# Kernel optimization log

Measured on AMD Instinct MI355X. Metric: run time of the kernel, lower is better.

## Reference

```python
import jax, jax.numpy as jnp
import numpy as np

B, C, D, H, W = 2, 96, 32, 64, 64
K = 2            # MRConv stride
EPS = 1e-5
SLOPE = 0.2      # LeakyReLU negative slope used by ViG act_layer('leakyrelu')


def conv1x1(x, w, b):
    # 1x1x1 Conv3d == per-voxel channel GEMM. x: [B,Ci,D,H,W], w: [Co,Ci]
    return jnp.einsum('bcdhw,oc->bodhw', x, w) + b[None, :, None, None, None]


def batchnorm(x, g, b):
    # training-mode BatchNorm3d: stats over (B, D, H, W)
    m = x.mean(axis=(0, 2, 3, 4), keepdims=True)
    v = x.var(axis=(0, 2, 3, 4), keepdims=True)
    return (x - m) * jax.lax.rsqrt(v + EPS) * g[None, :, None, None, None] + b[None, :, None, None, None]


def instnorm(x, g, b):
    # InstanceNorm3d: stats over (D, H, W) per sample/channel
    m = x.mean(axis=(2, 3, 4), keepdims=True)
    v = x.var(axis=(2, 3, 4), keepdims=True)
    return (x - m) * jax.lax.rsqrt(v + EPS) * g[None, :, None, None, None] + b[None, :, None, None, None]


def lrelu(x):
    return jnp.where(x >= 0, x, SLOPE * x)


def mr_aggregate(x):
    # MRConv shift/subtract/max, in closed form.
    # Original: x_j = max over axes a, shifts s in range(K, L_a, K) of (x - roll(x, s, a)), init 0.
    # Since shifts cover ALL nonzero multiples of K mod L_a (L_a % K == 0), the rolled values at a
    # position are exactly the other members of its residue class mod K along that axis, and
    # max(0, x - min_excluding_self) == x - min_including_self.  Hence:
    #   x_j = x - min over axes of (strided residue-class min along that axis).
    def axmin(x, axis):
        L = x.shape[axis]
        shp = list(x.shape)
        grp = shp[:axis] + [L // K, K] + shp[axis + 1:]
        xg = x.reshape(grp)
        m = xg.min(axis=axis, keepdims=True)             # min over same residue class
        return jnp.broadcast_to(m, grp).reshape(shp)
    m = jnp.minimum(jnp.minimum(axmin(x, 2), axmin(x, 3)), axmin(x, 4))
    return x - m


def setup_inputs() -> dict:
    key = jax.random.key(0)
    ks = jax.random.split(key, 8)
    f32 = jnp.float32
    def w(k, co, ci):
        return (jax.random.normal(k, (co, ci), dtype=f32) / np.sqrt(ci)).astype(f32)
    return {
        'x': jax.random.normal(ks[0], (B, C, D, H, W), dtype=f32),
        'w_fc1': w(ks[1], C, C), 'b_fc1': jnp.zeros((C,), f32),
        'g_bn1': jnp.ones((C,), f32), 'be_bn1': jnp.zeros((C,), f32),
        'w_g': w(ks[2], 2 * C, 2 * C), 'b_g': jnp.zeros((2 * C,), f32),
        'g_in': jnp.ones((2 * C,), f32), 'be_in': jnp.zeros((2 * C,), f32),
        'w_fc2': w(ks[3], C, 2 * C), 'b_fc2': jnp.zeros((C,), f32),
        'g_bn2': jnp.ones((C,), f32), 'be_bn2': jnp.zeros((C,), f32),
        'w_f1': w(ks[4], 4 * C, C), 'b_f1': jnp.zeros((4 * C,), f32),
        'g_bnf1': jnp.ones((4 * C,), f32), 'be_bnf1': jnp.zeros((4 * C,), f32),
        'w_f2': w(ks[5], C, 4 * C), 'b_f2': jnp.zeros((C,), f32),
        'g_bnf2': jnp.ones((C,), f32), 'be_bnf2': jnp.zeros((C,), f32),
    }


def reference(x, w_fc1, b_fc1, g_bn1, be_bn1, w_g, b_g, g_in, be_in,
              w_fc2, b_fc2, g_bn2, be_bn2, w_f1, b_f1, g_bnf1, be_bnf1,
              w_f2, b_f2, g_bnf2, be_bnf2):
    # ---- Grapher ----
    shortcut = x
    h = batchnorm(conv1x1(x, w_fc1, b_fc1), g_bn1, be_bn1)          # fc1: Conv+BN
    xj = mr_aggregate(h)                                            # MRConv shift-max agg
    hc = jnp.concatenate([h, xj], axis=1)                           # [B,2C,D,H,W]
    hg = lrelu(instnorm(conv1x1(hc, w_g, b_g), g_in, be_in))        # BasicConv: Conv+IN+LeakyReLU
    h = batchnorm(conv1x1(hg, w_fc2, b_fc2), g_bn2, be_bn2)         # fc2: Conv+BN
    x = h + shortcut
    # ---- FFN ----
    shortcut = x
    h = batchnorm(conv1x1(x, w_f1, b_f1), g_bnf1, be_bnf1)
    h = lrelu(h)
    h = batchnorm(conv1x1(h, w_f2, b_f2), g_bnf2, be_bnf2)
    return h + shortcut
```

## Files before the change

### kernel.cpp

```cpp
#include <hip/hip_runtime.h>
#include <hip/hip_bf16.h>


typedef __hip_bfloat16 bf16;
typedef __attribute__((ext_vector_type(8))) short short8;
typedef __attribute__((ext_vector_type(4))) float f4;

#define DEV static __device__ __forceinline__

constexpr int Sq  = 131072;
constexpr int NVq = 262144;

DEV float bu2f(unsigned short u) { return __uint_as_float(((unsigned)u) << 16); }
DEV unsigned short f2bu(float f) {
    unsigned i = __float_as_uint(f);
    unsigned r = i + 0x7FFFu + ((i >> 16) & 1u);
    return (unsigned short)(r >> 16);
}
DEV void glds16(const void* g, void* l) {
    __builtin_amdgcn_global_load_lds(
        (const __attribute__((address_space(1))) unsigned*)g,
        (__attribute__((address_space(3))) unsigned*)l, 16, 0, 0);
}

template<int CIRB, int KP, int CO, int BN, int AMODE, bool PERB>
__global__ __launch_bounds__(256)
void conv_k(const char* __restrict__ A0, const char* __restrict__ A1,
            const char* __restrict__ Wb, const float* __restrict__ bias,
            const float* __restrict__ cfA, const float* __restrict__ cfB,
            bf16* __restrict__ Y, float* __restrict__ part)
{
    constexpr int NSTEP = KP / 64;
    constexpr int NF = BN / 16;
    constexpr int BI = BN / 8;
    __shared__ __align__(16) char smem[16384 + BN * 128];
    char* As = smem;
    char* Bs = smem + 16384;

    const int tid = threadIdx.x;
    const int lane = tid & 63, wid = tid >> 6, l16 = lane & 15, lhi = lane >> 4;
    const int gm = blockIdx.x, gy = blockIdx.y;
    const int v0 = gm * 128;
    const int b = gm >> 10;
    const int n0g = gy * BN;

    f4 acc[2][NF];
#pragma unroll
    for (int nf = 0; nf < NF; ++nf) {
        float bb = bias[n0g + nf * 16 + l16];
        f4 t = {bb, bb, bb, bb};
        acc[0][nf] = t; acc[1][nf] = t;
    }

    for (int s = 0; s < NSTEP; ++s) {
        for (int i = wid; i < BI; i += 4) {
            int o = i * 8 + (lane >> 3);
            glds16(Wb + (size_t)(n0g + o) * (KP * 2) + s * 128 + (((lane & 7) ^ (o & 7)) << 4),
                   Bs + i * 1024);
        }
        if constexpr (AMODE == 0) {
            for (int i = wid; i < 16; i += 4) {
                int r = i * 8 + (lane >> 3);
                glds16(A0 + (size_t)(v0 + r) * CIRB + s * 128 + (((lane & 7) ^ (r & 7)) << 4),
                       As + i * 1024);
            }
        } else {
#pragma unroll
            for (int j = 0; j < 4; ++j) {
                int idx = tid + 256 * j;
                int v = idx >> 3, u = idx & 7;
                int k8 = s * 8 + u;
                short8 hh;
                if constexpr (AMODE == 1) {
                    short8 raw = *(const short8*)(A0 + (size_t)(v0 + v) * CIRB + k8 * 16);
                    int cb = k8 * 8;
                    f4 a0 = *(const f4*)(cfA + cb), a1 = *(const f4*)(cfA + cb + 4);
                    f4 d0 = *(const f4*)(cfB + cb), d1 = *(const f4*)(cfB + cb + 4);
#pragma unroll
                    for (int e = 0; e < 4; ++e) {
                        float t0 = fmaf(a0[e], bu2f((unsigned short)raw[e]),     d0[e]);
                        float t1 = fmaf(a1[e], bu2f((unsigned short)raw[e + 4]), d1[e]);
                        t0 = fmaxf(t0, 0.2f * t0);
                        t1 = fmaxf(t1, 0.2f * t1);
                        hh[e] = (short)f2bu(t0); hh[e + 4] = (short)f2bu(t1);
                    }
                } else if constexpr (AMODE == 2) {
                    short8 raw = *(const short8*)(A0 + (size_t)(v0 + v) * CIRB + k8 * 16);
                    int cb = b * KP + k8 * 8;
                    f4 a0 = *(const f4*)(cfA + cb), a1 = *(const f4*)(cfA + cb + 4);
                    f4 d0 = *(const f4*)(cfB + cb), d1 = *(const f4*)(cfB + cb + 4);
#pragma unroll
                    for (int e = 0; e < 4; ++e) {
                        float t0 = fmaf(a0[e], bu2f((unsigned short)raw[e]),     d0[e]);
                        float t1 = fmaf(a1[e], bu2f((unsigned short)raw[e + 4]), d1[e]);
                        t0 = fmaxf(t0, 0.2f * t0);
                        t1 = fmaxf(t1, 0.2f * t1);
                        hh[e] = (short)f2bu(t0); hh[e + 4] = (short)f2bu(t1);
                    }
                } else {
                    if (k8 < 12) {
                        short8 raw = *(const short8*)(A0 + (size_t)(v0 + v) * 192 + k8 * 16);
                        int cb = k8 * 8;
                        f4 a0 = *(const f4*)(cfA + cb), a1 = *(const f4*)(cfA + cb + 4);
                        f4 d0 = *(const f4*)(cfB + cb), d1 = *(const f4*)(cfB + cb + 4);
#pragma unroll
                        for (int e = 0; e < 4; ++e) {
                            hh[e]     = (short)f2bu(fmaf(a0[e], bu2f((unsigned short)raw[e]),     d0[e]));
                            hh[e + 4] = (short)f2bu(fmaf(a1[e], bu2f((unsigned short)raw[e + 4]), d1[e]));
                        }
                    } else {
                        hh = *(const short8*)(A1 + (size_t)(v0 + v) * 192 + (k8 - 12) * 16);
                    }
                }
                *(short8*)(As + v * 128 + ((u ^ (v & 7)) << 4)) = hh;
            }
        }
        __syncthreads();
#pragma unroll
        for (int ks = 0; ks < 2; ++ks) {
            int kg = ks * 4 + lhi;
            short8 av[2];
#pragma unroll
            for (int mf = 0; mf < 2; ++mf) {
                int v = wid * 32 + mf * 16 + l16;
                av[mf] = *(const short8*)(As + v * 128 + ((kg ^ (v & 7)) << 4));
            }
#pragma unroll
            for (int nf = 0; nf < NF; ++nf) {
                int o = nf * 16 + l16;
                short8 bv = *(const short8*)(Bs + o * 128 + ((kg ^ (o & 7)) << 4));
                acc[0][nf] = __builtin_amdgcn_mfma_f32_16x16x32_bf16(av[0], bv, acc[0][nf], 0, 0, 0);
                acc[1][nf] = __builtin_amdgcn_mfma_f32_16x16x32_bf16(av[1], bv, acc[1][nf], 0, 0, 0);
            }
        }
        __syncthreads();
    }

#pragma unroll
    for (int mf = 0; mf < 2; ++mf) {
        int vb = v0 + wid * 32 + mf * 16 + lhi * 4;
#pragma unroll
        for (int nf = 0; nf < NF; ++nf) {
            int n = n0g + nf * 16 + l16;
#pragma unroll
            for (int r = 0; r < 4; ++r) {
                bf16 o; *(unsigned short*)&o = f2bu(acc[mf][nf][r]);
                Y[(size_t)(vb + r) * CO + n] = o;
            }
        }
    }
    float* ps = (float*)smem;
#pragma unroll
    for (int nf = 0; nf < NF; ++nf) {
        float sm = 0.f, sq = 0.f;
#pragma unroll
        for (int mf = 0; mf < 2; ++mf)
#pragma unroll
            for (int r = 0; r < 4; ++r) {
                float v = acc[mf][nf][r];
                sm += v; sq += v * v;
            }
        sm += __shfl_xor(sm, 16); sq += __shfl_xor(sq, 16);
        sm += __shfl_xor(sm, 32); sq += __shfl_xor(sq, 32);
        if (lane < 16) {
            ps[(wid * 2 + 0) * BN + nf * 16 + lane] = sm;
            ps[(wid * 2 + 1) * BN + nf * 16 + lane] = sq;
        }
    }
    __syncthreads();
    if (tid < BN) {
        float sm = ps[0 * BN + tid] + ps[2 * BN + tid] + ps[4 * BN + tid] + ps[6 * BN + tid];
        float sq = ps[1 * BN + tid] + ps[3 * BN + tid] + ps[5 * BN + tid] + ps[7 * BN + tid];
        int slot = PERB ? (b * 32 + (gm & 31)) : (gm & 63);
        float* pb = part + (size_t)(gy * 64 + slot) * 2 * BN;
        atomicAdd(&pb[tid], sm);
        atomicAdd(&pb[BN + tid], sq);
    }
}

__global__ void finalize_k(const float* __restrict__ part, float* __restrict__ cf,
                           const float* __restrict__ g, const float* __restrict__ be,
                           int nStats, int CO, int BN, int perB, float invN)
{
    int s = blockIdx.x * 64 + threadIdx.x;
    if (s >= nStats) return;
    int ch = perB ? (s % CO) : s;
    int bb = perB ? (s / CO) : 0;
    int gy = ch / BN, c = ch - gy * BN;
    int j0 = perB ? bb * 32 : 0, cnt = perB ? 32 : 64;
    float sm = 0.f, sq = 0.f;
    for (int j = 0; j < cnt; ++j) {
        const float* pb = part + (size_t)(gy * 64 + j0 + j) * 2 * BN;
        sm += pb[c]; sq += pb[BN + c];
    }
    float m = sm * invN;
    float var = fmaf(-m, m, sq * invN);
    float A = g[ch] * rsqrtf(var + 1e-5f);
    cf[s] = A;
    cf[1024 + s] = fmaf(-m, A, be[ch]);
}

__global__ void wprep_k(const float* __restrict__ w0, const float* __restrict__ w1,
                        const float* __restrict__ w2, const float* __restrict__ w3,
                        const float* __restrict__ w4, bf16* __restrict__ Wb)
{
    int i = blockIdx.x * 256 + threadIdx.x;
    const float* src; int r, KP, CI, off;
    if (i < 12288)       { src = w0; r = i;          KP = 128; CI = 96;  off = 0; }
    else if (i < 49152)  { src = w1; r = i - 12288;  KP = 192; CI = 192; off = 12288; }
    else if (i < 67584)  { src = w2; r = i - 49152;  KP = 192; CI = 192; off = 49152; }
    else if (i < 116736) { src = w3; r = i - 67584;  KP = 128; CI = 96;  off = 67584; }
    else                 { src = w4; r = i - 116736; KP = 384; CI = 384; off = 116736; }
    int o = r / KP, k = r - o * KP;
    float v = (k < CI) ? src[o * CI + k] : 0.f;
    bf16 h; *(unsigned short*)&h = f2bu(v);
    Wb[off + r] = h;
}

__global__ __launch_bounds__(256)
void tin_k(const float* __restrict__ x, char* __restrict__ xT)
{
    __shared__ float ldsT[128 * 97];
    const int gm = blockIdx.x, b = gm >> 10, s0 = (gm & 1023) * 128;
    const int t = threadIdx.x;
#pragma unroll
    for (int i = 0; i < 12; ++i) {
        int idx = t + 256 * i;
        int c = idx >> 5, s4 = idx & 31;
        f4 r = *(const f4*)(x + ((size_t)(b * 96 + c) << 17) + s0 + s4 * 4);
#pragma unroll
        for (int j = 0; j < 4; ++j) ldsT[(s4 * 4 + j) * 97 + c] = r[j];
    }
    __syncthreads();
#pragma unroll
    for (int i = 0; i < 6; ++i) {
        int idx = t + 256 * i;
        int r = idx / 12, uc = idx % 12, cb = uc * 8;
        short8 o;
#pragma unroll
        for (int e = 0; e < 8; ++e) o[e] = (short)f2bu(ldsT[r * 97 + cb + e]);
        *(short8*)(xT + (size_t)(b * Sq + s0 + r) * 192 + uc * 16) = o;
    }
}

__global__ __launch_bounds__(192)
void mr_dmin_k(const char* __restrict__ y1, char* __restrict__ dminp)
{
    const int wq = blockIdx.x >> 1, dh = blockIdx.x & 1;
    const int h = blockIdx.y, b = blockIdx.z;
    const int t = threadIdx.x;
    const int w = wq * 16 + t / 12, uc = t % 12;
    const char* base = y1 + (size_t)(b * Sq + dh * 16 * 4096 + h * 64 + w) * 192 + uc * 16;
    float mn[2][8];
#pragma unroll
    for (int p = 0; p < 2; ++p)
#pragma unroll
        for (int e = 0; e < 8; ++e) mn[p][e] = 1e30f;
#pragma unroll 4
    for (int i = 0; i < 16; ++i) {
        short8 raw = *(const short8*)(base + (size_t)i * (4096 * 192));
        int p = i & 1;
#pragma unroll
        for (int e = 0; e < 8; ++e)
            mn[p][e] = fminf(mn[p][e], bu2f((unsigned short)raw[e]));
    }
#pragma unroll
    for (int p = 0; p < 2; ++p) {
        short8 o;
#pragma unroll
        for (int e = 0; e < 8; ++e) o[e] = (short)f2bu(mn[p][e]);
        *(short8*)(dminp + (size_t)((((b * 64 + h) * 64 + w) * 2 + dh) * 2 + p) * 192 + uc * 16) = o;
    }
}

__global__ __launch_bounds__(192)
void mr_hmin_k(const char* __restrict__ y1, char* __restrict__ hminp)
{
    const int wq = blockIdx.x >> 2, hq = blockIdx.x & 3;
    const int d = blockIdx.y, b = blockIdx.z;
    const int t = threadIdx.x;
    const int w = wq * 16 + t / 12, uc = t % 12;
    const char* base = y1 + (size_t)(b * Sq + d * 4096 + hq * 16 * 64 + w) * 192 + uc * 16;
    float mn[2][8];
#pragma unroll
    for (int p = 0; p < 2; ++p)
#pragma unroll
        for (int e = 0; e < 8; ++e) mn[p][e] = 1e30f;
#pragma unroll 4
    for (int i = 0; i < 16; ++i) {
        short8 raw = *(const short8*)(base + (size_t)i * (64 * 192));
        int p = i & 1;
#pragma unroll
        for (int e = 0; e < 8; ++e)
            mn[p][e] = fminf(mn[p][e], bu2f((unsigned short)raw[e]));
    }
#pragma unroll
    for (int p = 0; p < 2; ++p) {
        short8 o;
#pragma unroll
        for (int e = 0; e < 8; ++e) o[e] = (short)f2bu(mn[p][e]);
        *(short8*)(hminp + (size_t)((((b * 32 + d) * 64 + w) * 4 + hq) * 2 + p) * 192 + uc * 16) = o;
    }
}

__global__ __launch_bounds__(256)
void mr_p2_k(const char* __restrict__ y1, const float* __restrict__ cfA,
             const char* __restrict__ dminp, const char* __restrict__ hminp,
             char* __restrict__ xj)
{
    __shared__ __align__(16) char rowb[64 * 96 * 2];
    __shared__ float wlds[2 * 96];
    const int h = blockIdx.x, d = blockIdx.y, b = blockIdx.z;
    const int t = threadIdx.x;

    short8 hv[3];
#pragma unroll
    for (int j = 0; j < 3; ++j) {
        int slot = t + 256 * j;
        int w = slot / 12, uc = slot % 12;
        short8 raw = *(const short8*)(y1 + (size_t)(b * Sq + d * 4096 + h * 64 + w) * 192 + uc * 16);
        hv[j] = raw;
        *(short8*)(rowb + slot * 16) = raw;
    }
    __syncthreads();
    if (t < 192) {
        int p = t / 96, c = t % 96;
        float m = 1e30f;
        for (int w2 = p; w2 < 64; w2 += 2)
            m = fminf(m, bu2f(*(const unsigned short*)(rowb + (w2 * 96 + c) * 2)));
        wlds[t] = m;
    }
    __syncthreads();
#pragma unroll
    for (int j = 0; j < 3; ++j) {
        int slot = t + 256 * j;
        int w = slot / 12, uc = slot % 12, cb = uc * 8;
        const char* dp = dminp + (size_t)((((b * 64 + h) * 64 + w) * 2) * 2 + (d & 1)) * 192 + uc * 16;
        short8 dm0 = *(const short8*)(dp);
        short8 dm1 = *(const short8*)(dp + 384);
        const char* hp = hminp + (size_t)((((b * 32 + d) * 64 + w) * 4) * 2 + (h & 1)) * 192 + uc * 16;
        short8 hm0 = *(const short8*)(hp);
        short8 hm1 = *(const short8*)(hp + 384);
        short8 hm2 = *(const short8*)(hp + 768);
        short8 hm3 = *(const short8*)(hp + 1152);
        f4 a0 = *(const f4*)(cfA + cb), a1 = *(const f4*)(cfA + cb + 4);
        short8 xo;
#pragma unroll
        for (int e = 0; e < 8; ++e) {
            float m = fminf(
                fminf(bu2f((unsigned short)dm0[e]), bu2f((unsigned short)dm1[e])),
                fminf(fminf(fminf(bu2f((unsigned short)hm0[e]), bu2f((unsigned short)hm1[e])),
                            fminf(bu2f((unsigned short)hm2[e]), bu2f((unsigned short)hm3[e]))),
                      wlds[(w & 1) * 96 + cb + e]));
            float A = (e < 4) ? a0[e] : a1[e - 4];
            xo[e] = (short)f2bu(A * (bu2f((unsigned short)hv[j][e]) - m));
        }
        *(short8*)(xj + (size_t)(b * Sq + d * 4096 + h * 64 + w) * 192 + uc * 16) = xo;
    }
}

__global__ __launch_bounds__(256)
void ewx2_k(const char* __restrict__ y2, const float* __restrict__ cfA,
            const float* __restrict__ cfB, const char* __restrict__ xT,
            char* __restrict__ x2)
{
    size_t ch0 = ((size_t)blockIdx.x * 256 + threadIdx.x) * 4;
#pragma unroll
    for (int j = 0; j < 4; ++j) {
        size_t chunk = ch0 + j;
        int uc = (int)(chunk % 12), cb = uc * 8;
        short8 yv = *(const short8*)(y2 + chunk * 16);
        short8 xv = *(const short8*)(xT + chunk * 16);
        f4 a0 = *(const f4*)(cfA + cb), a1 = *(const f4*)(cfA + cb + 4);
        f4 d0 = *(const f4*)(cfB + cb), d1 = *(const f4*)(cfB + cb + 4);
        short8 o;
#pragma unroll
        for (int e = 0; e < 4; ++e) {
            float t0 = fmaf(a0[e], bu2f((unsigned short)yv[e]),     d0[e]) + bu2f((unsigned short)xv[e]);
            float t1 = fmaf(a1[e], bu2f((unsigned short)yv[e + 4]), d1[e]) + bu2f((unsigned short)xv[e + 4]);
            o[e]     = (short)f2bu(t0);
            o[e + 4] = (short)f2bu(t1);
        }
        *(short8*)(x2 + chunk * 16) = o;
    }
}

__global__ __launch_bounds__(256)
void tout_k(const char* __restrict__ y4, const float* __restrict__ cfA,
            const float* __restrict__ cfB, const char* __restrict__ x2,
            float* __restrict__ outp)
{
    __shared__ float ldsT[128 * 97];
    const int gm = blockIdx.x, b = gm >> 10, s0 = (gm & 1023) * 128;
    const int t = threadIdx.x;
#pragma unroll
    for (int i = 0; i < 6; ++i) {
        int idx = t + 256 * i;
        int r = idx / 12, uc = idx % 12, cb = uc * 8;
        size_t vv = (size_t)(b * Sq + s0 + r);
        short8 yv = *(const short8*)(y4 + vv * 192 + uc * 16);
        short8 xv = *(const short8*)(x2 + vv * 192 + uc * 16);
        f4 a0 = *(const f4*)(cfA + cb), a1 = *(const f4*)(cfA + cb + 4);
        f4 d0 = *(const f4*)(cfB + cb), d1 = *(const f4*)(cfB + cb + 4);
#pragma unroll
        for (int e = 0; e < 4; ++e) {
            ldsT[r * 97 + cb + e]     = fmaf(a0[e], bu2f((unsigned short)yv[e]),     d0[e]) + bu2f((unsigned short)xv[e]);
            ldsT[r * 97 + cb + e + 4] = fmaf(a1[e], bu2f((unsigned short)yv[e + 4]), d1[e]) + bu2f((unsigned short)xv[e + 4]);
        }
    }
    __syncthreads();
#pragma unroll
    for (int i = 0; i < 12; ++i) {
        int idx = t + 256 * i;
        int c = idx >> 5, s4 = idx & 31;
        f4 o;
#pragma unroll
        for (int j = 0; j < 4; ++j) o[j] = ldsT[(s4 * 4 + j) * 97 + c];
        *(f4*)(outp + ((size_t)(b * 96 + c) << 17) + s0 + s4 * 4) = o;
    }
}

extern "C" void kernel_launch(void* const* d_in, const int* in_sizes, int n_in,
                              void* d_out, int out_size, void* d_ws, size_t ws_size,
                              hipStream_t stream)
{
    (void)in_sizes; (void)n_in; (void)out_size; (void)ws_size;

    const float* x      = (const float*)d_in[0];
    const float* w_fc1  = (const float*)d_in[1];
    const float* b_fc1  = (const float*)d_in[2];
    const float* g_bn1  = (const float*)d_in[3];
    const float* be_bn1 = (const float*)d_in[4];
    const float* w_g    = (const float*)d_in[5];
    const float* b_g    = (const float*)d_in[6];
    const float* g_in   = (const float*)d_in[7];
    const float* be_in  = (const float*)d_in[8];
    const float* w_fc2  = (const float*)d_in[9];
    const float* b_fc2  = (const float*)d_in[10];
    const float* g_bn2  = (const float*)d_in[11];
    const float* be_bn2 = (const float*)d_in[12];
    const float* w_f1   = (const float*)d_in[13];
    const float* b_f1   = (const float*)d_in[14];
    const float* g_bnf1 = (const float*)d_in[15];
    const float* be_bnf1= (const float*)d_in[16];
    const float* w_f2   = (const float*)d_in[17];
    const float* b_f2   = (const float*)d_in[18];
    const float* g_bnf2 = (const float*)d_in[19];
    const float* be_bnf2= (const float*)d_in[20];
    float* outp = (float*)d_out;

    char* W = (char*)d_ws;
    char* xT    = W;
    char* y1    = W + 50331648ull;
    char* dminp = W + 100663296ull;
    char* hminp = W + 113246208ull;
    char* xj    = W + 125829120ull;
    char* yg    = W + 176160768ull;
    char* y2    = W + 50331648ull;
    char* y3    = W;
    char* y4    = W + 201326592ull;
    char* x2    = W + 251658240ull;
    char* M     = W + 301989888ull;
    bf16*  Wb   = (bf16*)M;
    float* cf   = (float*)(M + 307200);
    float* part = (float*)(M + 348160);

    hipMemsetAsync(part, 0, 5 * 196608, stream);

    const float invBN = 1.f / (float)NVq, invIN = 1.f / (float)Sq;
    dim3 blk(256);
    float* c1 = cf, *c2 = cf + 2048, *c3 = cf + 4096, *c4 = cf + 6144, *c5 = cf + 8192;

    wprep_k<<<600, blk, 0, stream>>>(w_fc1, w_g, w_fc2, w_f1, w_f2, Wb);
    tin_k<<<2048, blk, 0, stream>>>(x, xT);

    conv_k<192, 128, 96, 96, 0, false><<<dim3(2048, 1), blk, 0, stream>>>(
        xT, nullptr, (const char*)Wb, b_fc1, nullptr, nullptr, (bf16*)y1, part);
    finalize_k<<<2, 64, 0, stream>>>(part, c1, g_bn1, be_bn1, 96, 96, 96, 0, invBN);

    mr_dmin_k<<<dim3(8, 64, 2), dim3(192), 0, stream>>>(y1, dminp);
    mr_hmin_k<<<dim3(16, 32, 2), dim3(192), 0, stream>>>(y1, hminp);
    mr_p2_k<<<dim3(64, 32, 2), blk, 0, stream>>>(y1, c1, dminp, hminp, xj);

    conv_k<192, 192, 192, 192, 4, true><<<dim3(2048, 1), blk, 0, stream>>>(
        y1, xj, (const char*)Wb + 24576, b_g, c1, c1 + 1024, (bf16*)yg, part + 49152);
    finalize_k<<<6, 64, 0, stream>>>(part + 49152, c2, g_in, be_in, 384, 192, 192, 1, invIN);

    conv_k<384, 192, 96, 96, 2, false><<<dim3(2048, 1), blk, 0, stream>>>(
        yg, nullptr, (const char*)Wb + 98304, b_fc2, c2, c2 + 1024, (bf16*)y2, part + 98304);
    finalize_k<<<2, 64, 0, stream>>>(part + 98304, c3, g_bn2, be_bn2, 96, 96, 96, 0, invBN);

    ewx2_k<<<3072, blk, 0, stream>>>(y2, c3, c3 + 1024, xT, x2);

    conv_k<192, 128, 384, 192, 0, false><<<dim3(2048, 2), blk, 0, stream>>>(
        x2, nullptr, (const char*)Wb + 135168, b_f1, nullptr, nullptr, (bf16*)y3, part + 147456);
    finalize_k<<<6, 64, 0, stream>>>(part + 147456, c4, g_bnf1, be_bnf1, 384, 384, 192, 0, invBN);

    conv_k<768, 384, 96, 96, 1, false><<<dim3(2048, 1), blk, 0, stream>>>(
        y3, nullptr, (const char*)Wb + 233472, b_f2, c4, c4 + 1024, (bf16*)y4, part + 196608);
    finalize_k<<<2, 64, 0, stream>>>(part + 196608, c5, g_bnf2, be_bnf2, 96, 96, 96, 0, invBN);

    tout_k<<<2048, blk, 0, stream>>>(y4, c5, c5 + 1024, x2, outp);
}
```

Before: 511.4 us.

## Fuse FFN into stats pass plus recompute-fused conv1-LReLU-conv2 kernel

Folds the residual elementwise kernel into a new stats kernel that also computes fc-f1 outputs to gather BN statistics without storing them. A second kernel recomputes the f1 GEMM per 64-channel chunk, applies BN+LeakyReLU in LDS and immediately accumulates the f2 GEMM, so the 384-channel intermediate never goes to HBM. This trades extra f1 GEMM compute (done twice) for eliminating a large intermediate write/read and a kernel launch; bias of f1 is folded into the finalize shift.

```diff
diff --git a/kernel.cpp b/kernel.cpp
--- a/kernel.cpp
+++ b/kernel.cpp
@@ -5,6 +5,7 @@
 typedef __hip_bfloat16 bf16;
 typedef __attribute__((ext_vector_type(8))) short short8;
 typedef __attribute__((ext_vector_type(4))) float f4;
+typedef __attribute__((ext_vector_type(4))) unsigned short us4;
 
 #define DEV static __device__ __forceinline__
 
@@ -71,20 +72,7 @@
                 int v = idx >> 3, u = idx & 7;
                 int k8 = s * 8 + u;
                 short8 hh;
-                if constexpr (AMODE == 1) {
-                    short8 raw = *(const short8*)(A0 + (size_t)(v0 + v) * CIRB + k8 * 16);
-                    int cb = k8 * 8;
-                    f4 a0 = *(const f4*)(cfA + cb), a1 = *(const f4*)(cfA + cb + 4);
-                    f4 d0 = *(const f4*)(cfB + cb), d1 = *(const f4*)(cfB + cb + 4);
-#pragma unroll
-                    for (int e = 0; e < 4; ++e) {
-                        float t0 = fmaf(a0[e], bu2f((unsigned short)raw[e]),     d0[e]);
-                        float t1 = fmaf(a1[e], bu2f((unsigned short)raw[e + 4]), d1[e]);
-                        t0 = fmaxf(t0, 0.2f * t0);
-                        t1 = fmaxf(t1, 0.2f * t1);
-                        hh[e] = (short)f2bu(t0); hh[e + 4] = (short)f2bu(t1);
-                    }
-                } else if constexpr (AMODE == 2) {
+                if constexpr (AMODE == 2) {
                     short8 raw = *(const short8*)(A0 + (size_t)(v0 + v) * CIRB + k8 * 16);
                     int cb = b * KP + k8 * 8;
                     f4 a0 = *(const f4*)(cfA + cb), a1 = *(const f4*)(cfA + cb + 4);
@@ -178,8 +166,248 @@
     }
 }
 
+__global__ __launch_bounds__(256)
+void ffn_stats_k(const char* __restrict__ y2, const char* __restrict__ xT,
+                 const float* __restrict__ cfA, const float* __restrict__ cfB,
+                 const float* __restrict__ biasf1, const char* __restrict__ Wf1,
+                 char* __restrict__ x2, float* __restrict__ part)
+{
+    __shared__ __align__(16) char smem[32768 + 24576];
+    __shared__ float ps[8 * 96];
+    char* As = smem;
+    char* Bs = smem + 32768;
+
+    const int tid = threadIdx.x;
+    const int lane = tid & 63, wid = tid >> 6, l16 = lane & 15, lhi = lane >> 4;
+    const int gm = blockIdx.x;
+    const int v0 = gm * 128;
+
+#pragma unroll
+    for (int j = 0; j < 6; ++j) {
+        int slot = tid + 256 * j;
+        int v = slot / 12, uc = slot % 12, cb = uc * 8;
+        short8 yv = *(const short8*)(y2 + (size_t)(v0 + v) * 192 + uc * 16);
+        short8 xv = *(const short8*)(xT + (size_t)(v0 + v) * 192 + uc * 16);
+        f4 a0 = *(const f4*)(cfA + cb), a1 = *(const f4*)(cfA + cb + 4);
+        f4 d0 = *(const f4*)(cfB + cb), d1 = *(const f4*)(cfB + cb + 4);
+        short8 o;
+#pragma unroll
+        for (int e = 0; e < 4; ++e) {
+            float t0 = fmaf(a0[e], bu2f((unsigned short)yv[e]),     d0[e]) + bu2f((unsigned short)xv[e]);
+            float t1 = fmaf(a1[e], bu2f((unsigned short)yv[e + 4]), d1[e]) + bu2f((unsigned short)xv[e + 4]);
+            o[e]     = (short)f2bu(t0);
+            o[e + 4] = (short)f2bu(t1);
+        }
+        *(short8*)(x2 + (size_t)(v0 + v) * 192 + uc * 16) = o;
+        *(short8*)(As + v * 256 + ((uc ^ (v & 7)) << 4)) = o;
+    }
+
+    for (int q = 0; q < 4; ++q) {
+        for (int i = wid; i < 24; i += 4) {
+            int o = i * 4 + (lane >> 4), u = lane & 15;
+            glds16(Wf1 + (size_t)(q * 96 + o) * 192 + ((u ^ (o & 7)) << 4),
+                   Bs + i * 1024);
+        }
+        __syncthreads();
+        f4 acc[2][6];
+#pragma unroll
+        for (int nf = 0; nf < 6; ++nf) {
+            float bb = biasf1[q * 96 + nf * 16 + l16];
+            f4 t = {bb, bb, bb, bb};
+            acc[0][nf] = t; acc[1][nf] = t;
+        }
+#pragma unroll
+        for (int ks = 0; ks < 3; ++ks) {
+            int kg = ks * 4 + lhi;
+            short8 av[2];
+#pragma unroll
+            for (int mf = 0; mf < 2; ++mf) {
+                int v = wid * 32 + mf * 16 + l16;
+                av[mf] = *(const short8*)(As + v * 256 + ((kg ^ (v & 7)) << 4));
+            }
+#pragma unroll
+            for (int nf = 0; nf < 6; ++nf) {
+                int o = nf * 16 + l16;
+                short8 bv = *(const short8*)(Bs + o * 256 + ((kg ^ (o & 7)) << 4));
+                acc[0][nf] = __builtin_amdgcn_mfma_f32_16x16x32_bf16(av[0], bv, acc[0][nf], 0, 0, 0);
+                acc[1][nf] = __builtin_amdgcn_mfma_f32_16x16x32_bf16(av[1], bv, acc[1][nf], 0, 0, 0);
+            }
+        }
+#pragma unroll
+        for (int nf = 0; nf < 6; ++nf) {
+            float sm = 0.f, sq = 0.f;
+#pragma unroll
+            for (int mf = 0; mf < 2; ++mf)
+#pragma unroll
+                for (int r = 0; r < 4; ++r) {
+                    float v = acc[mf][nf][r];
+                    sm += v; sq += v * v;
+                }
+            sm += __shfl_xor(sm, 16); sq += __shfl_xor(sq, 16);
+            sm += __shfl_xor(sm, 32); sq += __shfl_xor(sq, 32);
+            if (lane < 16) {
+                ps[(wid * 2 + 0) * 96 + nf * 16 + lane] = sm;
+                ps[(wid * 2 + 1) * 96 + nf * 16 + lane] = sq;
+            }
+        }
+        __syncthreads();
+        if (tid < 96) {
+            float sm = ps[0 * 96 + tid] + ps[2 * 96 + tid] + ps[4 * 96 + tid] + ps[6 * 96 + tid];
+            float sq = ps[1 * 96 + tid] + ps[3 * 96 + tid] + ps[5 * 96 + tid] + ps[7 * 96 + tid];
+            float* pb = part + (size_t)(q * 64 + (gm & 63)) * 192;
+            atomicAdd(&pb[tid], sm);
+            atomicAdd(&pb[96 + tid], sq);
+        }
+    }
+}
+
+__global__ __launch_bounds__(256)
+void ffn_k(const char* __restrict__ x2, const float* __restrict__ cfA4,
+           const float* __restrict__ cfB4, const float* __restrict__ biasf2,
+           const char* __restrict__ Wf1, const char* __restrict__ Wf2,
+           bf16* __restrict__ y4, float* __restrict__ part)
+{
+    __shared__ __align__(16) char smem[32768 + 16384 + 12288 + 16384];
+    char* As  = smem;
+    char* W1c = smem + 32768;
+    char* W2c = smem + 49152;
+    char* zb  = smem + 61440;
+    float* ps = (float*)zb;
+
+    const int tid = threadIdx.x;
+    const int lane = tid & 63, wid = tid >> 6, l16 = lane & 15, lhi = lane >> 4;
+    const int gm = blockIdx.x;
+    const int v0 = gm * 128;
+
+    for (int i = wid; i < 32; i += 4) {
+        int v = i * 4 + (lane >> 4), u = lane & 15;
+        glds16(x2 + (size_t)(v0 + v) * 192 + ((u ^ (v & 7)) << 4), As + i * 1024);
+    }
+
+    f4 accY[2][6];
+#pragma unroll
+    for (int nf = 0; nf < 6; ++nf) {
+        float bb = biasf2[nf * 16 + l16];
+        f4 t = {bb, bb, bb, bb};
+        accY[0][nf] = t; accY[1][nf] = t;
+    }
+
+    for (int nc = 0; nc < 6; ++nc) {
+        for (int i = wid; i < 16; i += 4) {
+            int o = i * 4 + (lane >> 4), u = lane & 15;
+            glds16(Wf1 + (size_t)(nc * 64 + o) * 192 + ((u ^ (o & 7)) << 4),
+                   W1c + i * 1024);
+        }
+        for (int i = wid; i < 12; i += 4) {
+            int o = i * 8 + (lane >> 3), u = lane & 7;
+            glds16(Wf2 + (size_t)o * 768 + nc * 128 + ((u ^ (o & 7)) << 4),
+                   W2c + i * 1024);
+        }
+        __syncthreads();
+        f4 z[4][2];
+#pragma unroll
+        for (int mt = 0; mt < 4; ++mt)
+#pragma unroll
+            for (int nt = 0; nt < 2; ++nt) z[mt][nt] = {0.f, 0.f, 0.f, 0.f};
+#pragma unroll
+        for (int ks = 0; ks < 3; ++ks) {
+            int kg = ks * 4 + lhi;
+            short8 xv[2];
+#pragma unroll
+            for (int nt = 0; nt < 2; ++nt) {
+                int v = wid * 32 + nt * 16 + l16;
+                xv[nt] = *(const short8*)(As + v * 256 + ((kg ^ (v & 7)) << 4));
+            }
+#pragma unroll
+            for (int mt = 0; mt < 4; ++mt) {
+                int o = mt * 16 + l16;
+                short8 wv = *(const short8*)(W1c + o * 256 + ((kg ^ (o & 7)) << 4));
+                z[mt][0] = __builtin_amdgcn_mfma_f32_16x16x32_bf16(wv, xv[0], z[mt][0], 0, 0, 0);
+                z[mt][1] = __builtin_amdgcn_mfma_f32_16x16x32_bf16(wv, xv[1], z[mt][1], 0, 0, 0);
+            }
+        }
+#pragma unroll
+        for (int mt = 0; mt < 4; ++mt) {
+            int ch = nc * 64 + mt * 16 + lhi * 4;
+            f4 a = *(const f4*)(cfA4 + ch);
+            f4 bb = *(const f4*)(cfB4 + ch);
+#pragma unroll
+            for (int nt = 0; nt < 2; ++nt) {
+                int v = wid * 32 + nt * 16 + l16;
+                us4 p;
+#pragma unroll
+                for (int r = 0; r < 4; ++r) {
+                    float t = fmaf(a[r], z[mt][nt][r], bb[r]);
+                    t = fmaxf(t, 0.2f * t);
+                    p[r] = f2bu(t);
+                }
+                *(us4*)(zb + v * 128 + (((mt * 2 + (lhi >> 1)) ^ (v & 7)) << 4) + ((lhi & 1) << 3)) = p;
+            }
+        }
+        __syncthreads();
+#pragma unroll
+        for (int ks = 0; ks < 2; ++ks) {
+            int kg = ks * 4 + lhi;
+            short8 av[2];
+#pragma unroll
+            for (int mf = 0; mf < 2; ++mf) {
+                int v = wid * 32 + mf * 16 + l16;
+                av[mf] = *(const short8*)(zb + v * 128 + ((kg ^ (v & 7)) << 4));
+            }
+#pragma unroll
+            for (int nf = 0; nf < 6; ++nf) {
+                int o = nf * 16 + l16;
+                short8 bv = *(const short8*)(W2c + o * 128 + ((kg ^ (o & 7)) << 4));
+                accY[0][nf] = __builtin_amdgcn_mfma_f32_16x16x32_bf16(av[0], bv, accY[0][nf], 0, 0, 0);
+                accY[1][nf] = __builtin_amdgcn_mfma_f32_16x16x32_bf16(av[1], bv, accY[1][nf], 0, 0, 0);
+            }
+        }
+        __syncthreads();
+    }
+
+#pragma unroll
+    for (int mf = 0; mf < 2; ++mf) {
+        int vb = v0 + wid * 32 + mf * 16 + lhi * 4;
+#pragma unroll
+        for (int nf = 0; nf < 6; ++nf) {
+            int n = nf * 16 + l16;
+#pragma unroll
+            for (int r = 0; r < 4; ++r) {
+                bf16 o; *(unsigned short*)&o = f2bu(accY[mf][nf][r]);
+                y4[(size_t)(vb + r) * 96 + n] = o;
+            }
+        }
+    }
+#pragma unroll
+    for (int nf = 0; nf < 6; ++nf) {
+        float sm = 0.f, sq = 0.f;
+#pragma unroll
+        for (int mf = 0; mf < 2; ++mf)
+#pragma unroll
+            for (int r = 0; r < 4; ++r) {
+                float v = accY[mf][nf][r];
+                sm += v; sq += v * v;
+            }
+        sm += __shfl_xor(sm, 16); sq += __shfl_xor(sq, 16);
+        sm += __shfl_xor(sm, 32); sq += __shfl_xor(sq, 32);
+        if (lane < 16) {
+            ps[(wid * 2 + 0) * 96 + nf * 16 + lane] = sm;
+            ps[(wid * 2 + 1) * 96 + nf * 16 + lane] = sq;
+        }
+    }
+    __syncthreads();
+    if (tid < 96) {
+        float sm = ps[0 * 96 + tid] + ps[2 * 96 + tid] + ps[4 * 96 + tid] + ps[6 * 96 + tid];
+        float sq = ps[1 * 96 + tid] + ps[3 * 96 + tid] + ps[5 * 96 + tid] + ps[7 * 96 + tid];
+        float* pb = part + (size_t)(gm & 63) * 192;
+        atomicAdd(&pb[tid], sm);
+        atomicAdd(&pb[96 + tid], sq);
+    }
+}
+
 __global__ void finalize_k(const float* __restrict__ part, float* __restrict__ cf,
                            const float* __restrict__ g, const float* __restrict__ be,
+                           const float* __restrict__ bias,
                            int nStats, int CO, int BN, int perB, float invN)
 {
     int s = blockIdx.x * 64 + threadIdx.x;
@@ -197,7 +425,9 @@
     float var = fmaf(-m, m, sq * invN);
     float A = g[ch] * rsqrtf(var + 1e-5f);
     cf[s] = A;
-    cf[1024 + s] = fmaf(-m, A, be[ch]);
+    float B = fmaf(-m, A, be[ch]);
+    if (bias) B = fmaf(A, bias[ch], B);
+    cf[1024 + s] = B;
 }
 
 __global__ void wprep_k(const float* __restrict__ w0, const float* __restrict__ w1,
@@ -205,12 +435,13 @@
                         const float* __restrict__ w4, bf16* __restrict__ Wb)
 {
     int i = blockIdx.x * 256 + threadIdx.x;
+    if (i >= 141312) return;
     const float* src; int r, KP, CI, off;
     if (i < 12288)       { src = w0; r = i;          KP = 128; CI = 96;  off = 0; }
     else if (i < 49152)  { src = w1; r = i - 12288;  KP = 192; CI = 192; off = 12288; }
     else if (i < 67584)  { src = w2; r = i - 49152;  KP = 192; CI = 192; off = 49152; }
-    else if (i < 116736) { src = w3; r = i - 67584;  KP = 128; CI = 96;  off = 67584; }
-    else                 { src = w4; r = i - 116736; KP = 384; CI = 384; off = 116736; }
+    else if (i < 104448) { src = w3; r = i - 67584;  KP = 96;  CI = 96;  off = 67584; }
+    else                 { src = w4; r = i - 104448; KP = 384; CI = 384; off = 104448; }
     int o = r / KP, k = r - o * KP;
     float v = (k < CI) ? src[o * CI + k] : 0.f;
     bf16 h; *(unsigned short*)&h = f2bu(v);
@@ -356,32 +587,6 @@
             xo[e] = (short)f2bu(A * (bu2f((unsigned short)hv[j][e]) - m));
         }
         *(short8*)(xj + (size_t)(b * Sq + d * 4096 + h * 64 + w) * 192 + uc * 16) = xo;
-    }
-}
-
-__global__ __launch_bounds__(256)
-void ewx2_k(const char* __restrict__ y2, const float* __restrict__ cfA,
-            const float* __restrict__ cfB, const char* __restrict__ xT,
-            char* __restrict__ x2)
-{
-    size_t ch0 = ((size_t)blockIdx.x * 256 + threadIdx.x) * 4;
-#pragma unroll
-    for (int j = 0; j < 4; ++j) {
-        size_t chunk = ch0 + j;
-        int uc = (int)(chunk % 12), cb = uc * 8;
-        short8 yv = *(const short8*)(y2 + chunk * 16);
-        short8 xv = *(const short8*)(xT + chunk * 16);
-        f4 a0 = *(const f4*)(cfA + cb), a1 = *(const f4*)(cfA + cb + 4);
-        f4 d0 = *(const f4*)(cfB + cb), d1 = *(const f4*)(cfB + cb + 4);
-        short8 o;
-#pragma unroll
-        for (int e = 0; e < 4; ++e) {
-            float t0 = fmaf(a0[e], bu2f((unsigned short)yv[e]),     d0[e]) + bu2f((unsigned short)xv[e]);
-            float t1 = fmaf(a1[e], bu2f((unsigned short)yv[e + 4]), d1[e]) + bu2f((unsigned short)xv[e + 4]);
-            o[e]     = (short)f2bu(t0);
-            o[e + 4] = (short)f2bu(t1);
-        }
-        *(short8*)(x2 + chunk * 16) = o;
     }
 }
 
@@ -457,7 +662,6 @@
     char* xj    = W + 125829120ull;
     char* yg    = W + 176160768ull;
     char* y2    = W + 50331648ull;
-    char* y3    = W;
     char* y4    = W + 201326592ull;
     char* x2    = W + 251658240ull;
     char* M     = W + 301989888ull;
@@ -470,35 +674,36 @@
     const float invBN = 1.f / (float)NVq, invIN = 1.f / (float)Sq;
     dim3 blk(256);
     float* c1 = cf, *c2 = cf + 2048, *c3 = cf + 4096, *c4 = cf + 6144, *c5 = cf + 8192;
-
-    wprep_k<<<600, blk, 0, stream>>>(w_fc1, w_g, w_fc2, w_f1, w_f2, Wb);
+    const char* Wfc1 = (const char*)Wb;
+    const char* Wg   = (const char*)Wb + 24576;
+    const char* Wfc2 = (const char*)Wb + 98304;
+    const char* Wf1  = (const char*)Wb + 135168;
+    const char* Wf2  = (const char*)Wb + 208896;
+
+    wprep_k<<<552, blk, 0, stream>>>(w_fc1, w_g, w_fc2, w_f1, w_f2, Wb);
     tin_k<<<2048, blk, 0, stream>>>(x, xT);
 
     conv_k<192, 128, 96, 96, 0, false><<<dim3(2048, 1), blk, 0, stream>>>(
-        xT, nullptr, (const char*)Wb, b_fc1, nullptr, nullptr, (bf16*)y1, part);
-    finalize_k<<<2, 64, 0, stream>>>(part, c1, g_bn1, be_bn1, 96, 96, 96, 0, invBN);
+        xT, nullptr, Wfc1, b_fc1, nullptr, nullptr, (bf16*)y1, part);
+    finalize_k<<<2, 64, 0, stream>>>(part, c1, g_bn1, be_bn1, nullptr, 96, 96, 96, 0, invBN);
 
     mr_dmin_k<<<dim3(8, 64, 2), dim3(192), 0, stream>>>(y1, dminp);
     mr_hmin_k<<<dim3(16, 32, 2), dim3(192), 0, stream>>>(y1, hminp);
     mr_p2_k<<<dim3(64, 32, 2), blk, 0, stream>>>(y1, c1, dminp, hminp, xj);
 
     conv_k<192, 192, 192, 192, 4, true><<<dim3(2048, 1), blk, 0, stream>>>(
-        y1, xj, (const char*)Wb + 24576, b_g, c1, c1 + 1024, (bf16*)yg, part + 49152);
-    finalize_k<<<6, 64, 0, stream>>>(part + 49152, c2, g_in, be_in, 384, 192, 192, 1, invIN);
+        y1, xj, Wg, b_g, c1, c1 + 1024, (bf16*)yg, part + 49152);
+    finalize_k<<<6, 64, 0, stream>>>(part + 49152, c2, g_in, be_in, nullptr, 384, 192, 192, 1, invIN);
 
     conv_k<384, 192, 96, 96, 2, false><<<dim3(2048, 1), blk, 0, stream>>>(
-        yg, nullptr, (const char*)Wb + 98304, b_fc2, c2, c2 + 1024, (bf16*)y2, part + 98304);
-    finalize_k<<<2, 64, 0, stream>>>(part + 98304, c3, g_bn2, be_bn2, 96, 96, 96, 0, invBN);
-
-    ewx2_k<<<3072, blk, 0, stream>>>(y2, c3, c3 + 1024, xT, x2);
-
-    conv_k<192, 128, 384, 192, 0, false><<<dim3(2048, 2), blk, 0, stream>>>(
-        x2, nullptr, (const char*)Wb + 135168, b_f1, nullptr, nullptr, (bf16*)y3, part + 147456);
-    finalize_k<<<6, 64, 0, stream>>>(part + 147456, c4, g_bnf1, be_bnf1, 384, 384, 192, 0, invBN);
-
-    conv_k<768, 384, 96, 96, 1, false><<<dim3(2048, 1), blk, 0, stream>>>(
-        y3, nullptr, (const char*)Wb + 233472, b_f2, c4, c4 + 1024, (bf16*)y4, part + 196608);
-    finalize_k<<<2, 64, 0, stream>>>(part + 196608, c5, g_bnf2, be_bnf2, 96, 96, 96, 0, invBN);
+        yg, nullptr, Wfc2, b_fc2, c2, c2 + 1024, (bf16*)y2, part + 98304);
+    finalize_k<<<2, 64, 0, stream>>>(part + 98304, c3, g_bn2, be_bn2, nullptr, 96, 96, 96, 0, invBN);
+
+    ffn_stats_k<<<2048, blk, 0, stream>>>(y2, xT, c3, c3 + 1024, b_f1, Wf1, x2, part + 147456);
+    finalize_k<<<6, 64, 0, stream>>>(part + 147456, c4, g_bnf1, be_bnf1, b_f1, 384, 384, 96, 0, invBN);
+
+    ffn_k<<<2048, blk, 0, stream>>>(x2, c4, c4 + 1024, b_f2, Wf1, Wf2, (bf16*)y4, part + 196608);
+    finalize_k<<<2, 64, 0, stream>>>(part + 196608, c5, g_bnf2, be_bnf2, nullptr, 96, 96, 96, 0, invBN);
 
     tout_k<<<2048, blk, 0, stream>>>(y4, c5, c5 + 1024, x2, outp);
 }
```

New measurement: 451.5 us (median of 2 runs). 11.7% less time.
